# Performance work log

Hardware: AMD Instinct MI355X
Metric: run time of the kernel (lower is better)

## Reference

```python
import jax, jax.numpy as jnp
import numpy as np

B, S, H, I, E, TOP_K = 16, 2048, 768, 3072, 8, 2


def setup_inputs() -> dict:
    key = jax.random.key(0)
    ks = jax.random.split(key, 5)
    scaled = lambda k, shape, fan_in: jax.random.normal(k, shape, jnp.float32) * (fan_in ** -0.5)
    return {
        "hidden_states": jax.random.normal(ks[0], (B, S, H), jnp.float32),
        "gate_w": scaled(ks[1], (E, H), H),          # router: nn.Linear(H, E, bias=False)
        "w1": scaled(ks[2], (E, H, I), H),            # expert intermediate.dense
        "b1": jnp.zeros((E, I), jnp.float32),
        "w2": scaled(ks[3], (E, I, H), I),            # expert output.dense
        "b2": jnp.zeros((E, H), jnp.float32),
    }


def reference(hidden_states, gate_w, w1, b1, w2, b2):
    b, s, h = hidden_states.shape
    e = gate_w.shape[0]
    x = hidden_states.reshape(-1, h)  # [T, H], T = B*S
    # Router
    router_logits = x @ gate_w.T  # [T, E]
    probs = jax.nn.softmax(router_logits.astype(jnp.float32), axis=-1)
    rw, sel = jax.lax.top_k(probs, TOP_K)  # [T, top_k]
    rw = rw / rw.sum(axis=-1, keepdims=True)
    rw = rw.astype(x.dtype)
    # Dense combine weights: zero for unselected experts (equivalent to the
    # gather/index_add dispatch in the torch code, full-capacity no-drop MoE).
    combine = (jax.nn.one_hot(sel, e, dtype=x.dtype) * rw[..., None]).sum(axis=1)  # [T, E]
    out = jnp.zeros_like(x)
    for ei in range(e):  # fixed small expert loop
        hmid = jax.nn.gelu(x @ w1[ei] + b1[ei], approximate=False)  # [T, I]
        y = hmid @ w2[ei] + b2[ei]  # [T, H] (dropout is identity in eval)
        out = out + combine[:, ei:ei + 1] * y
    return out.reshape(b, s, h), router_logits
```

## Files before the change

### kernel.cpp

```cpp
#include <hip/hip_runtime.h>
#include <hip/hip_bf16.h>
#include <math.h>
#include <stdint.h>

#define T_TOK 32768
#define H_DIM 768
#define I_DIM 3072
#define E_NUM 8
#define PADROWS 66560
#define NTILE   520

typedef __attribute__((ext_vector_type(8))) __bf16 bf16x8;
typedef __attribute__((ext_vector_type(4))) float floatx4;

__device__ inline __bf16 f2bf(float f) { return (__bf16)f; }
__device__ inline unsigned short f2bfu(float f) {
    __bf16 b = (__bf16)f; return *(unsigned short*)&b;
}
__device__ inline float bfu2f(unsigned short u) {
    union { unsigned v; float f; } c; c.v = ((unsigned)u) << 16; return c.f;
}

__device__ inline void g2lds16(const void* g, void* l) {
    __builtin_amdgcn_global_load_lds(
        (const __attribute__((address_space(1))) unsigned int*)g,
        (__attribute__((address_space(3))) unsigned int*)l, 16, 0, 0);
}

__device__ inline float gelu_fast(float x) {
    float x2 = x * x;
    float t = x * (0.7978845608f + 0.0356774081f * x2);
    float e = __expf(-2.f * t);
    return x / (1.f + e);
}

__global__ __launch_bounds__(256) void router_kernel(
    const float* __restrict__ x, const float* __restrict__ gw,
    float* __restrict__ logits, int* __restrict__ tok_sel,
    float* __restrict__ tok_w, int* __restrict__ cnt)
{
    __shared__ float sgw[E_NUM * H_DIM];
    __shared__ int lcnt[E_NUM];
    int tid = threadIdx.x;
    for (int i = tid; i < E_NUM * H_DIM; i += 256) sgw[i] = gw[i];
    if (tid < E_NUM) lcnt[tid] = 0;
    __syncthreads();

    int t = blockIdx.x * 256 + tid;
    const float* xr = x + (size_t)t * H_DIM;
    float acc[E_NUM];
#pragma unroll
    for (int e = 0; e < E_NUM; e++) acc[e] = 0.f;
    for (int k = 0; k < H_DIM; k += 4) {
        float4 xv = *(const float4*)(xr + k);
#pragma unroll
        for (int e = 0; e < E_NUM; e++) {
            const float* g = &sgw[e * H_DIM + k];
            acc[e] += xv.x * g[0] + xv.y * g[1] + xv.z * g[2] + xv.w * g[3];
        }
    }
#pragma unroll
    for (int e = 0; e < E_NUM; e++) logits[(size_t)t * E_NUM + e] = acc[e];

    int e1 = 0; float v1 = acc[0];
#pragma unroll
    for (int e = 1; e < E_NUM; e++) if (acc[e] > v1) { v1 = acc[e]; e1 = e; }
    int e2 = (e1 == 0) ? 1 : 0; float v2 = acc[(e1 == 0) ? 1 : 0];
#pragma unroll
    for (int e = 0; e < E_NUM; e++)
        if (e != e1 && acc[e] > v2) { v2 = acc[e]; e2 = e; }

    float p2 = expf(v2 - v1);
    float s = 1.f + p2;
    tok_sel[2 * t] = e1; tok_sel[2 * t + 1] = e2;
    tok_w[2 * t] = 1.f / s; tok_w[2 * t + 1] = p2 / s;

    atomicAdd(&lcnt[e1], 1); atomicAdd(&lcnt[e2], 1);
    __syncthreads();
    if (tid < E_NUM) atomicAdd(&cnt[tid], lcnt[tid]);
}

__global__ void scan_kernel(const int* __restrict__ cnt, int* __restrict__ off)
{
    if (threadIdx.x == 0 && blockIdx.x == 0) {
        int o = 0;
        for (int e = 0; e < E_NUM; e++) {
            off[e] = o;
            o += (cnt[e] + 127) & ~127;
        }
        off[E_NUM] = o;
    }
}

__global__ __launch_bounds__(256) void scatter_kernel(
    const int* __restrict__ tok_sel, const float* __restrict__ tok_w,
    const int* __restrict__ off, int* __restrict__ fill,
    int* __restrict__ pair_token, float* __restrict__ pair_w,
    int* __restrict__ tok_pos)
{
    __shared__ int lcnt[E_NUM];
    __shared__ int base[E_NUM];
    int tid = threadIdx.x;
    if (tid < E_NUM) lcnt[tid] = 0;
    __syncthreads();
    int t = blockIdx.x * 256 + tid;
    int e1 = tok_sel[2 * t], e2 = tok_sel[2 * t + 1];
    int lp1 = atomicAdd(&lcnt[e1], 1);
    int lp2 = atomicAdd(&lcnt[e2], 1);
    __syncthreads();
    if (tid < E_NUM) base[tid] = (lcnt[tid] > 0) ? atomicAdd(&fill[tid], lcnt[tid]) : 0;
    __syncthreads();
    int p1 = off[e1] + base[e1] + lp1;
    int p2 = off[e2] + base[e2] + lp2;
    pair_token[p1] = t; pair_w[p1] = tok_w[2 * t];
    pair_token[p2] = t; pair_w[p2] = tok_w[2 * t + 1];
    tok_pos[2 * t] = p1; tok_pos[2 * t + 1] = p2;
}

__global__ __launch_bounds__(256) void convert_x(
    const float* __restrict__ x, __bf16* __restrict__ xb)
{
    int i = blockIdx.x * 256 + threadIdx.x;
    float4 a = ((const float4*)x)[2 * i];
    float4 b = ((const float4*)x)[2 * i + 1];
    bf16x8 o;
    o[0] = f2bf(a.x); o[1] = f2bf(a.y); o[2] = f2bf(a.z); o[3] = f2bf(a.w);
    o[4] = f2bf(b.x); o[5] = f2bf(b.y); o[6] = f2bf(b.z); o[7] = f2bf(b.w);
    ((bf16x8*)xb)[i] = o;
}

__global__ __launch_bounds__(256) void transpose_w(
    const float* __restrict__ W, __bf16* __restrict__ Wt, int R, int C)
{
    __shared__ unsigned short T[64][66];
    int e = blockIdx.z;
    int r0 = blockIdx.y * 64, c0 = blockIdx.x * 64;
    const float* Wp = W + (size_t)e * R * C;
    __bf16* Wtp = Wt + (size_t)e * C * R;
    int tid = threadIdx.x;

    int rl = tid >> 2, cg = tid & 3;
    const float* src = Wp + (size_t)(r0 + rl) * C + c0 + cg * 16;
#pragma unroll
    for (int u = 0; u < 4; u++) {
        float4 v = *(const float4*)(src + u * 4);
        unsigned p0 = (unsigned)f2bfu(v.x) | ((unsigned)f2bfu(v.y) << 16);
        unsigned p1 = (unsigned)f2bfu(v.z) | ((unsigned)f2bfu(v.w) << 16);
        *(unsigned*)&T[rl][cg * 16 + u * 4]     = p0;
        *(unsigned*)&T[rl][cg * 16 + u * 4 + 2] = p1;
    }
    __syncthreads();

    int cl = tid >> 2, rg = tid & 3;
    __bf16* dst = Wtp + (size_t)(c0 + cl) * R + r0 + rg * 16;
#pragma unroll
    for (int half = 0; half < 2; half++) {
        bf16x8 o;
#pragma unroll
        for (int j = 0; j < 8; j++) {
            unsigned short b = T[rg * 16 + half * 8 + j][cl];
            o[j] = *(__bf16*)&b;
        }
        *(bf16x8*)(dst + half * 8) = o;
    }
}

__global__ __launch_bounds__(256) void moe_gemm1(
    const __bf16* __restrict__ xbf, const __bf16* __restrict__ w1t,
    const float* __restrict__ b1, const int* __restrict__ off_g,
    const int* __restrict__ pair_token, __bf16* __restrict__ hmid,
    int chunk_base, int chunkI, int r0)
{
    __shared__ __align__(16) __bf16 As[128][32];
    __shared__ __align__(16) __bf16 Bs[128][32];
    int m0 = r0 + blockIdx.x * 128;
    if (m0 >= off_g[E_NUM]) return;
    int e = 0;
#pragma unroll
    for (int k = 0; k < E_NUM - 1; k++) if (m0 >= off_g[k + 1]) e = k + 1;

    int tid = threadIdx.x;
    int w = tid >> 6, lane = tid & 63;
    int ln = lane & 15, q = lane >> 4;
    int wm = w >> 1, wn = w & 1;
    int sub = lane >> 2, kp = lane & 3;
    int i0 = chunk_base + blockIdx.y * 128;

    int rA0 = m0 + w * 32 + sub;
    int t0 = pair_token[rA0]; if (t0 < 0) t0 = 0;
    int t1 = pair_token[rA0 + 16]; if (t1 < 0) t1 = 0;
    const __bf16* gA0 = xbf + (size_t)t0 * H_DIM + kp * 8;
    const __bf16* gA1 = xbf + (size_t)t1 * H_DIM + kp * 8;
    const __bf16* gB0 = w1t + ((size_t)e * I_DIM + i0 + w * 32 + sub) * H_DIM + kp * 8;
    const __bf16* gB1 = gB0 + (size_t)16 * H_DIM;
    void* lA0 = &As[w * 32][0];
    void* lA1 = &As[w * 32 + 16][0];
    void* lB0 = &Bs[w * 32][0];
    void* lB1 = &Bs[w * 32 + 16][0];

    floatx4 acc[4][4];
#pragma unroll
    for (int a = 0; a < 4; a++)
#pragma unroll
        for (int b = 0; b < 4; b++) acc[a][b] = (floatx4){0.f, 0.f, 0.f, 0.f};

    for (int kk = 0; kk < H_DIM; kk += 32) {
        __syncthreads();
        g2lds16(gA0 + kk, lA0);
        g2lds16(gA1 + kk, lA1);
        g2lds16(gB0 + kk, lB0);
        g2lds16(gB1 + kk, lB1);
        __syncthreads();
        bf16x8 af[4], bfr[4];
#pragma unroll
        for (int mt = 0; mt < 4; mt++) af[mt] = *(bf16x8*)&As[wm * 64 + mt * 16 + ln][q * 8];
#pragma unroll
        for (int nt = 0; nt < 4; nt++) bfr[nt] = *(bf16x8*)&Bs[wn * 64 + nt * 16 + ln][q * 8];
#pragma unroll
        for (int mt = 0; mt < 4; mt++)
#pragma unroll
            for (int nt = 0; nt < 4; nt++)
                acc[mt][nt] = __builtin_amdgcn_mfma_f32_16x16x32_bf16(af[mt], bfr[nt], acc[mt][nt], 0, 0, 0);
    }

#pragma unroll
    for (int nt = 0; nt < 4; nt++) {
        int colg = i0 + wn * 64 + nt * 16 + ln;
        float bv = b1[e * I_DIM + colg];
        int coll = colg - chunk_base;
#pragma unroll
        for (int mt = 0; mt < 4; mt++)
#pragma unroll
            for (int r = 0; r < 4; r++) {
                int row = m0 + wm * 64 + mt * 16 + q * 4 + r;
                float v = acc[mt][nt][r] + bv;
                hmid[(size_t)(row - r0) * chunkI + coll] = f2bf(gelu_fast(v));
            }
    }
}

__global__ __launch_bounds__(256) void moe_gemm2_y(
    const __bf16* __restrict__ hmid, const __bf16* __restrict__ w2t,
    const int* __restrict__ off_g, __bf16* __restrict__ y_pair, int r0)
{
    __shared__ __align__(16) __bf16 As[128][32];
    __shared__ __align__(16) __bf16 Bs[128][32];
    int m0 = r0 + blockIdx.x * 128;
    if (m0 >= off_g[E_NUM]) return;
    int e = 0;
#pragma unroll
    for (int k = 0; k < E_NUM - 1; k++) if (m0 >= off_g[k + 1]) e = k + 1;

    int tid = threadIdx.x;
    int w = tid >> 6, lane = tid & 63;
    int ln = lane & 15, q = lane >> 4;
    int wm = w >> 1, wn = w & 1;
    int sub = lane >> 2, kp = lane & 3;
    int h0 = blockIdx.y * 128;

    const __bf16* gA0 = hmid + (size_t)(m0 - r0 + w * 32 + sub) * I_DIM + kp * 8;
    const __bf16* gA1 = gA0 + (size_t)16 * I_DIM;
    const __bf16* gB0 = w2t + ((size_t)e * H_DIM + h0 + w * 32 + sub) * I_DIM + kp * 8;
    const __bf16* gB1 = gB0 + (size_t)16 * I_DIM;
    void* lA0 = &As[w * 32][0];
    void* lA1 = &As[w * 32 + 16][0];
    void* lB0 = &Bs[w * 32][0];
    void* lB1 = &Bs[w * 32 + 16][0];

    floatx4 acc[4][4];
#pragma unroll
    for (int a = 0; a < 4; a++)
#pragma unroll
        for (int b = 0; b < 4; b++) acc[a][b] = (floatx4){0.f, 0.f, 0.f, 0.f};

    for (int kk = 0; kk < I_DIM; kk += 32) {
        __syncthreads();
        g2lds16(gA0 + kk, lA0);
        g2lds16(gA1 + kk, lA1);
        g2lds16(gB0 + kk, lB0);
        g2lds16(gB1 + kk, lB1);
        __syncthreads();
        bf16x8 af[4], bfr[4];
#pragma unroll
        for (int mt = 0; mt < 4; mt++) af[mt] = *(bf16x8*)&As[wm * 64 + mt * 16 + ln][q * 8];
#pragma unroll
        for (int nt = 0; nt < 4; nt++) bfr[nt] = *(bf16x8*)&Bs[wn * 64 + nt * 16 + ln][q * 8];
#pragma unroll
        for (int mt = 0; mt < 4; mt++)
#pragma unroll
            for (int nt = 0; nt < 4; nt++)
                acc[mt][nt] = __builtin_amdgcn_mfma_f32_16x16x32_bf16(af[mt], bfr[nt], acc[mt][nt], 0, 0, 0);
    }

#pragma unroll
    for (int mt = 0; mt < 4; mt++)
#pragma unroll
        for (int r = 0; r < 4; r++) {
            int row = m0 + wm * 64 + mt * 16 + q * 4 + r;
            __bf16* yrow = y_pair + (size_t)row * H_DIM + h0 + wn * 64;
#pragma unroll
            for (int nt = 0; nt < 4; nt++)
                yrow[nt * 16 + ln] = f2bf(acc[mt][nt][r]);
        }
}

__global__ __launch_bounds__(256) void combine_kernel(
    const __bf16* __restrict__ y_pair, const int* __restrict__ tok_pos,
    const int* __restrict__ tok_sel, const float* __restrict__ tok_w,
    const float* __restrict__ b2, float* __restrict__ out)
{
    int g = blockIdx.x * 256 + threadIdx.x;
    int t = g / 192;
    int u = g - t * 192;
    int p1 = tok_pos[2 * t], p2 = tok_pos[2 * t + 1];
    int e1 = tok_sel[2 * t], e2 = tok_sel[2 * t + 1];
    float w1 = tok_w[2 * t], w2 = tok_w[2 * t + 1];
    ushort4 a = *(const ushort4*)(y_pair + (size_t)p1 * H_DIM + u * 4);
    ushort4 b = *(const ushort4*)(y_pair + (size_t)p2 * H_DIM + u * 4);
    float4 ba = *(const float4*)(b2 + e1 * H_DIM + u * 4);
    float4 bb = *(const float4*)(b2 + e2 * H_DIM + u * 4);
    float4 o;
    o.x = w1 * (bfu2f(a.x) + ba.x) + w2 * (bfu2f(b.x) + bb.x);
    o.y = w1 * (bfu2f(a.y) + ba.y) + w2 * (bfu2f(b.y) + bb.y);
    o.z = w1 * (bfu2f(a.z) + ba.z) + w2 * (bfu2f(b.z) + bb.z);
    o.w = w1 * (bfu2f(a.w) + ba.w) + w2 * (bfu2f(b.w) + bb.w);
    *(float4*)(out + (size_t)t * H_DIM + u * 4) = o;
}

__global__ __launch_bounds__(256) void moe_gemm2_atomic(
    const __bf16* __restrict__ hmid, const __bf16* __restrict__ w2t,
    const float* __restrict__ b2, const int* __restrict__ off_g,
    const int* __restrict__ pair_token, const float* __restrict__ pair_w,
    float* __restrict__ out, int chunk_base, int chunkI)
{
    __shared__ __align__(16) __bf16 As[128][32];
    __shared__ __align__(16) __bf16 Bs[128][32];
    int m0 = blockIdx.x * 128;
    if (m0 >= off_g[E_NUM]) return;
    int e = 0;
#pragma unroll
    for (int k = 0; k < E_NUM - 1; k++) if (m0 >= off_g[k + 1]) e = k + 1;

    int tid = threadIdx.x;
    int w = tid >> 6, lane = tid & 63;
    int ln = lane & 15, q = lane >> 4;
    int wm = w >> 1, wn = w & 1;
    int sub = lane >> 2, kp = lane & 3;
    int h0 = blockIdx.y * 128;

    const __bf16* gA0 = hmid + (size_t)(m0 + w * 32 + sub) * chunkI + kp * 8;
    const __bf16* gA1 = gA0 + (size_t)16 * chunkI;
    const __bf16* gB0 = w2t + ((size_t)e * H_DIM + h0 + w * 32 + sub) * I_DIM + chunk_base + kp * 8;
    const __bf16* gB1 = gB0 + (size_t)16 * I_DIM;
    void* lA0 = &As[w * 32][0];
    void* lA1 = &As[w * 32 + 16][0];
    void* lB0 = &Bs[w * 32][0];
    void* lB1 = &Bs[w * 32 + 16][0];

    floatx4 acc[4][4];
#pragma unroll
    for (int a = 0; a < 4; a++)
#pragma unroll
        for (int b = 0; b < 4; b++) acc[a][b] = (floatx4){0.f, 0.f, 0.f, 0.f};

    for (int kk = 0; kk < chunkI; kk += 32) {
        __syncthreads();
        g2lds16(gA0 + kk, lA0);
        g2lds16(gA1 + kk, lA1);
        g2lds16(gB0 + kk, lB0);
        g2lds16(gB1 + kk, lB1);
        __syncthreads();
        bf16x8 af[4], bfr[4];
#pragma unroll
        for (int mt = 0; mt < 4; mt++) af[mt] = *(bf16x8*)&As[wm * 64 + mt * 16 + ln][q * 8];
#pragma unroll
        for (int nt = 0; nt < 4; nt++) bfr[nt] = *(bf16x8*)&Bs[wn * 64 + nt * 16 + ln][q * 8];
#pragma unroll
        for (int mt = 0; mt < 4; mt++)
#pragma unroll
            for (int nt = 0; nt < 4; nt++)
                acc[mt][nt] = __builtin_amdgcn_mfma_f32_16x16x32_bf16(af[mt], bfr[nt], acc[mt][nt], 0, 0, 0);
    }

    float bscale = (chunk_base == 0) ? 1.f : 0.f;
    float bv[4];
#pragma unroll
    for (int nt = 0; nt < 4; nt++) bv[nt] = bscale * b2[e * H_DIM + h0 + wn * 64 + nt * 16 + ln];

#pragma unroll
    for (int mt = 0; mt < 4; mt++)
#pragma unroll
        for (int r = 0; r < 4; r++) {
            int row = m0 + wm * 64 + mt * 16 + q * 4 + r;
            int tok = pair_token[row];
            if (tok < 0) continue;
            float pw = pair_w[row];
            float* orow = out + (size_t)tok * H_DIM + h0 + wn * 64;
#pragma unroll
            for (int nt = 0; nt < 4; nt++) {
                float v = (acc[mt][nt][r] + bv[nt]) * pw;
                atomicAdd(orow + nt * 16 + ln, v);
            }
        }
}

extern "C" void kernel_launch(void* const* d_in, const int* in_sizes, int n_in,
                              void* d_out, int out_size, void* d_ws, size_t ws_size,
                              hipStream_t stream)
{
    const float* x  = (const float*)d_in[0];
    const float* gw = (const float*)d_in[1];
    const float* w1 = (const float*)d_in[2];
    const float* b1 = (const float*)d_in[3];
    const float* w2 = (const float*)d_in[4];
    const float* b2 = (const float*)d_in[5];
    float* out = (float*)d_out;
    float* logits = out + (size_t)T_TOK * H_DIM;

    const size_t XBF_SZ = (size_t)T_TOK * H_DIM * 2;
    const size_t W1T_SZ = (size_t)E_NUM * H_DIM * I_DIM * 2;
    const size_t W2T_SZ = W1T_SZ;
    const size_t YP_SZ  = (size_t)PADROWS * H_DIM * 2;

    char* p0 = (char*)d_ws;
    char* p = p0;
    int* cnt  = (int*)p; p += 32;
    int* fill = (int*)p; p += 32;
    int* off  = (int*)p; p += 64;
    int* tok_sel = (int*)p;  p += (size_t)2 * T_TOK * 4;
    float* tok_w = (float*)p; p += (size_t)2 * T_TOK * 4;
    int* tok_pos = (int*)p;  p += (size_t)2 * T_TOK * 4;
    int* pair_token = (int*)p;  p += (size_t)PADROWS * 4;
    float* pair_w   = (float*)p; p += (size_t)PADROWS * 4;
    p = (char*)(((uintptr_t)p + 255) & ~(uintptr_t)255);

    __bf16* xbf = (__bf16*)p;
    __bf16* w1t = (__bf16*)(p + XBF_SZ);
    __bf16* w2t = (__bf16*)(p + XBF_SZ + W1T_SZ);
    char* after_w = p + XBF_SZ + W1T_SZ + W2T_SZ;

    size_t base_fused = (size_t)(after_w - p0) + YP_SZ;
    long long avail_f = (long long)ws_size - (long long)base_fused;
    int mrows = 0;
    if (avail_f >= (long long)128 * I_DIM * 2) {
        long long r = avail_f / ((long long)I_DIM * 2);
        if (r > PADROWS) r = PADROWS;
        mrows = (int)(r & ~127LL);
    }
    bool fused = (mrows >= 128);

    hipMemsetAsync(cnt, 0, 128, stream);
    hipMemsetAsync(pair_token, 0xFF, (size_t)PADROWS * 4, stream);

    router_kernel<<<T_TOK / 256, 256, 0, stream>>>(x, gw, logits, tok_sel, tok_w, cnt);
    scan_kernel<<<1, 64, 0, stream>>>(cnt, off);
    scatter_kernel<<<T_TOK / 256, 256, 0, stream>>>(tok_sel, tok_w, off, fill,
                                                    pair_token, pair_w, tok_pos);

    convert_x<<<(T_TOK * H_DIM / 8) / 256, 256, 0, stream>>>(x, xbf);
    transpose_w<<<dim3(I_DIM / 64, H_DIM / 64, E_NUM), 256, 0, stream>>>(w1, w1t, H_DIM, I_DIM);
    transpose_w<<<dim3(H_DIM / 64, I_DIM / 64, E_NUM), 256, 0, stream>>>(w2, w2t, I_DIM, H_DIM);

    if (fused) {
        __bf16* y_pair = (__bf16*)after_w;
        __bf16* hmid = (__bf16*)(after_w + YP_SZ);

        for (int r0 = 0; r0 < PADROWS; r0 += mrows) {
            int rows = PADROWS - r0; if (rows > mrows) rows = mrows;
            int xt = rows / 128;
            moe_gemm1<<<dim3(xt, I_DIM / 128), 256, 0, stream>>>(
                xbf, w1t, b1, off, pair_token, hmid, 0, I_DIM, r0);
            moe_gemm2_y<<<dim3(xt, H_DIM / 128), 256, 0, stream>>>(
                hmid, w2t, off, y_pair, r0);
        }
        combine_kernel<<<(T_TOK * 192) / 256, 256, 0, stream>>>(
            y_pair, tok_pos, tok_sel, tok_w, b2, out);
    } else {
        char* hm = after_w;
        size_t avail = (ws_size > (size_t)(hm - p0)) ? ws_size - (size_t)(hm - p0) : 0;
        static const int cands[] = {3072, 1536, 1024, 768, 512, 384, 256, 128};
        int chunkI = 128;
        for (int i = 0; i < 8; i++)
            if ((size_t)PADROWS * (size_t)cands[i] * 2 <= avail) { chunkI = cands[i]; break; }
        __bf16* hmid = (__bf16*)hm;

        hipMemsetAsync(out, 0, (size_t)T_TOK * H_DIM * sizeof(float), stream);
        for (int cb = 0; cb < I_DIM; cb += chunkI) {
            moe_gemm1<<<dim3(NTILE, chunkI / 128), 256, 0, stream>>>(
                xbf, w1t, b1, off, pair_token, hmid, cb, chunkI, 0);
            moe_gemm2_atomic<<<dim3(NTILE, H_DIM / 128), 256, 0, stream>>>(
                hmid, w2t, b2, off, pair_token, pair_w, out, cb, chunkI);
        }
    }
}
```

Before: 1.494 ms.

## Stage GEMM epilogues through LDS for coalesced stores and cap row chunk size

```diff
diff --git a/kernel.cpp b/kernel.cpp
--- a/kernel.cpp
+++ b/kernel.cpp
@@ -9,6 +9,7 @@
 #define E_NUM 8
 #define PADROWS 66560
 #define NTILE   520
+#define MROWS_CAP 12288
 
 typedef __attribute__((ext_vector_type(8))) __bf16 bf16x8;
 typedef __attribute__((ext_vector_type(4))) float floatx4;
@@ -171,8 +172,10 @@
     const int* __restrict__ pair_token, __bf16* __restrict__ hmid,
     int chunk_base, int chunkI, int r0)
 {
-    __shared__ __align__(16) __bf16 As[128][32];
-    __shared__ __align__(16) __bf16 Bs[128][32];
+    __shared__ __align__(16) __bf16 smem[8704];
+    __bf16 (*As)[32] = (__bf16(*)[32])smem;
+    __bf16 (*Bs)[32] = (__bf16(*)[32])(smem + 4096);
+
     int m0 = r0 + blockIdx.x * 128;
     if (m0 >= off_g[E_NUM]) return;
     int e = 0;
@@ -223,19 +226,33 @@
                 acc[mt][nt] = __builtin_amdgcn_mfma_f32_16x16x32_bf16(af[mt], bfr[nt], acc[mt][nt], 0, 0, 0);
     }
 
-#pragma unroll
-    for (int nt = 0; nt < 4; nt++) {
-        int colg = i0 + wn * 64 + nt * 16 + ln;
-        float bv = b1[e * I_DIM + colg];
-        int coll = colg - chunk_base;
-#pragma unroll
-        for (int mt = 0; mt < 4; mt++)
-#pragma unroll
-            for (int r = 0; r < 4; r++) {
-                int row = m0 + wm * 64 + mt * 16 + q * 4 + r;
-                float v = acc[mt][nt][r] + bv;
-                hmid[(size_t)(row - r0) * chunkI + coll] = f2bf(gelu_fast(v));
-            }
+    float bv[4];
+#pragma unroll
+    for (int nt = 0; nt < 4; nt++) bv[nt] = b1[e * I_DIM + i0 + wn * 64 + nt * 16 + ln];
+
+    __bf16 (*Ls)[136] = (__bf16(*)[136])smem;
+    __syncthreads();
+    int rl = tid >> 2, qtr = tid & 3;
+#pragma unroll
+    for (int phase = 0; phase < 2; phase++) {
+        if (wm == phase) {
+#pragma unroll
+            for (int nt = 0; nt < 4; nt++)
+#pragma unroll
+                for (int mt = 0; mt < 4; mt++)
+#pragma unroll
+                    for (int r = 0; r < 4; r++)
+                        Ls[mt * 16 + q * 4 + r][wn * 64 + nt * 16 + ln] =
+                            f2bf(gelu_fast(acc[mt][nt][r] + bv[nt]));
+        }
+        __syncthreads();
+        int grow = m0 + phase * 64 + rl;
+        __bf16* d = hmid + (size_t)(grow - r0) * chunkI + (i0 - chunk_base) + qtr * 32;
+        const __bf16* s = &Ls[rl][qtr * 32];
+#pragma unroll
+        for (int j = 0; j < 4; j++)
+            ((bf16x8*)d)[j] = *(const bf16x8*)(s + j * 8);
+        __syncthreads();
     }
 }
 
@@ -243,8 +260,10 @@
     const __bf16* __restrict__ hmid, const __bf16* __restrict__ w2t,
     const int* __restrict__ off_g, __bf16* __restrict__ y_pair, int r0)
 {
-    __shared__ __align__(16) __bf16 As[128][32];
-    __shared__ __align__(16) __bf16 Bs[128][32];
+    __shared__ __align__(16) __bf16 smem[8704];
+    __bf16 (*As)[32] = (__bf16(*)[32])smem;
+    __bf16 (*Bs)[32] = (__bf16(*)[32])(smem + 4096);
+
     int m0 = r0 + blockIdx.x * 128;
     if (m0 >= off_g[E_NUM]) return;
     int e = 0;
@@ -292,16 +311,30 @@
                 acc[mt][nt] = __builtin_amdgcn_mfma_f32_16x16x32_bf16(af[mt], bfr[nt], acc[mt][nt], 0, 0, 0);
     }
 
-#pragma unroll
-    for (int mt = 0; mt < 4; mt++)
-#pragma unroll
-        for (int r = 0; r < 4; r++) {
-            int row = m0 + wm * 64 + mt * 16 + q * 4 + r;
-            __bf16* yrow = y_pair + (size_t)row * H_DIM + h0 + wn * 64;
+    __bf16 (*Ls)[136] = (__bf16(*)[136])smem;
+    __syncthreads();
+    int rl = tid >> 2, qtr = tid & 3;
+#pragma unroll
+    for (int phase = 0; phase < 2; phase++) {
+        if (wm == phase) {
 #pragma unroll
             for (int nt = 0; nt < 4; nt++)
-                yrow[nt * 16 + ln] = f2bf(acc[mt][nt][r]);
-        }
+#pragma unroll
+                for (int mt = 0; mt < 4; mt++)
+#pragma unroll
+                    for (int r = 0; r < 4; r++)
+                        Ls[mt * 16 + q * 4 + r][wn * 64 + nt * 16 + ln] =
+                            f2bf(acc[mt][nt][r]);
+        }
+        __syncthreads();
+        int grow = m0 + phase * 64 + rl;
+        __bf16* d = y_pair + (size_t)grow * H_DIM + h0 + qtr * 32;
+        const __bf16* s = &Ls[rl][qtr * 32];
+#pragma unroll
+        for (int j = 0; j < 4; j++)
+            ((bf16x8*)d)[j] = *(const bf16x8*)(s + j * 8);
+        __syncthreads();
+    }
 }
 
 __global__ __launch_bounds__(256) void combine_kernel(
@@ -442,12 +475,13 @@
     size_t base_fused = (size_t)(after_w - p0) + YP_SZ;
     long long avail_f = (long long)ws_size - (long long)base_fused;
     int mrows = 0;
-    if (avail_f >= (long long)128 * I_DIM * 2) {
+    if (avail_f > 0) {
         long long r = avail_f / ((long long)I_DIM * 2);
         if (r > PADROWS) r = PADROWS;
         mrows = (int)(r & ~127LL);
     }
-    bool fused = (mrows >= 128);
+    if (mrows > MROWS_CAP) mrows = MROWS_CAP;
+    bool fused = (mrows >= 2048);
 
     hipMemsetAsync(cnt, 0, 128, stream);
     hipMemsetAsync(pair_token, 0xFF, (size_t)PADROWS * 4, stream);
```

Result: slower. 1.579 ms (+5.7%).
